# Kernel optimization log

Hardware: AMD Instinct MI355X
Metric: run time of the kernel (lower is better)

## Reference

```python
import jax, jax.numpy as jnp
import numpy as np

EMBED_DIM = 1024
HEAD_DIM = 128


def setup_inputs() -> dict:
    key = jax.random.key(0)
    k_x, k_qkv, k_out, k_b = jax.random.split(key, 4)
    x = jax.random.normal(k_x, (4, 4096, EMBED_DIM), dtype=jnp.float32)
    # torch Linear weights, stored as [in, out] so y = x @ W
    w_qkv = jax.random.normal(k_qkv, (EMBED_DIM, 3 * HEAD_DIM), dtype=jnp.float32) * (EMBED_DIM ** -0.5)
    w_out = jax.random.normal(k_out, (HEAD_DIM, EMBED_DIM), dtype=jnp.float32) * (HEAD_DIM ** -0.5)
    b_out = jax.random.normal(k_b, (EMBED_DIM,), dtype=jnp.float32) * 0.01
    return {"x": x, "w_qkv": w_qkv, "w_out": w_out, "b_out": b_out}


def reference(x, w_qkv, w_out, b_out):
    b, t, c = x.shape
    qkv = x @ w_qkv                                  # [b, t, 3*head_dim]
    q, k, v = jnp.split(qkv, 3, axis=-1)             # each [b, t, head_dim]
    # NOTE: original scales by embed_dim**-0.5 (c), not head_dim**-0.5
    wei = jnp.einsum('bqd,bkd->bqk', q, k) * (c ** -0.5)  # [b, t, t]
    causal = jnp.tril(jnp.ones((t, t), dtype=bool))
    wei = jnp.where(causal, wei, -jnp.inf)
    wei = jax.nn.softmax(wei, axis=-1)
    out = jnp.einsum('bqk,bkd->bqd', wei, v)         # [b, t, head_dim]
    return out @ w_out + b_out                       # [b, t, embed_dim]
```

## Files before the change

kernel.cpp:

```cpp
#include <hip/hip_runtime.h>
#include <hip/hip_bf16.h>

typedef __attribute__((ext_vector_type(8))) short short8;
typedef __attribute__((ext_vector_type(4))) float float4v;

#define AS1(p) ((const __attribute__((address_space(1))) void*)(p))
#define AS3(p) ((__attribute__((address_space(3))) void*)(p))

#define NSPLIT 8

__device__ __forceinline__ ushort f2bf(float f) {
    union { float f; unsigned u; } v; v.f = f;
    unsigned u = v.u;
    unsigned r = (u + 0x7fffu + ((u >> 16) & 1u)) >> 16;
    return (ushort)r;
}
__device__ __forceinline__ ushort f2bf_trunc(float f) {
    union { float f; unsigned u; } v; v.f = f;
    return (ushort)(v.u >> 16);
}
__device__ __forceinline__ float bf2f(ushort u) {
    union { unsigned u; float f; } v; v.u = ((unsigned)u) << 16;
    return v.f;
}

__global__ void transpose_cast(const float* __restrict__ in, ushort* __restrict__ out, int R, int C) {
    int idx = blockIdx.x * blockDim.x + threadIdx.x;
    if (idx >= R * C) return;
    int r = idx / C, c = idx - r * C;
    out[(size_t)c * R + r] = f2bf(in[idx]);
}

__device__ __forceinline__ void stage128x64(const ushort* gbase, int ld, ushort* lds, int tid) {
    const int wavebase = tid & 192;
#pragma unroll
    for (int j = 0; j < 4; ++j) {
        int idx = j * 256 + tid;
        int row = idx >> 3;
        int slot = idx & 7;
        int s = slot ^ (row & 7);
        const ushort* g = gbase + (size_t)row * ld + s * 8;
        int ldsoff = (j * 256 + wavebase) * 16;
        __builtin_amdgcn_global_load_lds(AS1(g), AS3((char*)lds + ldsoff), 16, 0, 0);
    }
}

__device__ __forceinline__ void compute64(const ushort* As, const ushort* Bs,
                                          int wr, int wc, int row16, int grp,
                                          float4v acc[4][4]) {
    const char* Ab = (const char*)As;
    const char* Bb = (const char*)Bs;
#pragma unroll
    for (int kk = 0; kk < 2; ++kk) {
        short8 a[4], b[4];
        const int sw = row16 & 7;
#pragma unroll
        for (int m = 0; m < 4; ++m)
            a[m] = *(const short8*)(Ab + (wr * 64 + m * 16 + row16) * 128 + (((kk * 4 + grp) ^ sw) << 4));
#pragma unroll
        for (int n = 0; n < 4; ++n)
            b[n] = *(const short8*)(Bb + (wc * 64 + n * 16 + row16) * 128 + (((kk * 4 + grp) ^ sw) << 4));
#pragma unroll
        for (int m = 0; m < 4; ++m)
#pragma unroll
            for (int n = 0; n < 4; ++n)
                acc[m][n] = __builtin_amdgcn_mfma_f32_16x16x32_bf16(a[m], b[n], acc[m][n], 0, 0, 0);
    }
}

__device__ __forceinline__ void compute64x128(const ushort* As, const ushort* Bs,
                                              int wr, int wc, int row16, int grp,
                                              float4v acc[2][4]) {
    const char* Ab = (const char*)As;
    const char* Bb = (const char*)Bs;
#pragma unroll
    for (int kk = 0; kk < 2; ++kk) {
        short8 a[2], b[4];
        const int sw = row16 & 7;
#pragma unroll
        for (int m = 0; m < 2; ++m)
            a[m] = *(const short8*)(Ab + (wr * 32 + m * 16 + row16) * 128 + (((kk * 4 + grp) ^ sw) << 4));
#pragma unroll
        for (int n = 0; n < 4; ++n)
            b[n] = *(const short8*)(Bb + (wc * 64 + n * 16 + row16) * 128 + (((kk * 4 + grp) ^ sw) << 4));
#pragma unroll
        for (int m = 0; m < 2; ++m)
#pragma unroll
            for (int n = 0; n < 4; ++n)
                acc[m][n] = __builtin_amdgcn_mfma_f32_16x16x32_bf16(a[m], b[n], acc[m][n], 0, 0, 0);
    }
}

__global__ __launch_bounds__(256) void gemm_qkv(const float* __restrict__ x,
                                                const ushort* __restrict__ wT,
                                                ushort* __restrict__ Qm,
                                                ushort* __restrict__ Km,
                                                ushort* __restrict__ Vt) {
    __shared__ ushort S[12288];
    ushort* As = S;
    ushort* Bs = S + 4096;
    const int tid = threadIdx.x;
    const int lane = tid & 63, w = tid >> 6;
    const int row16 = lane & 15, grp = lane >> 4;
    const int wr = w >> 1, wc = w & 1;
    const int mt = blockIdx.x * 64;
    const int by = blockIdx.y;
    const int n0 = by * 128;

    float4v acc[2][4];
#pragma unroll
    for (int m = 0; m < 2; ++m)
#pragma unroll
        for (int n = 0; n < 4; ++n) acc[m][n] = (float4v){0.f, 0.f, 0.f, 0.f};

#define LOAD_A(KT)                                                         \
    _Pragma("unroll") for (int j = 0; j < 2; ++j) {                        \
        int idx = j * 256 + tid;                                           \
        int row = idx >> 3, slot = idx & 7;                                \
        const float* src = x + (size_t)(mt + row) * 1024 + (KT) + slot * 8;\
        va[j][0] = *(const float4*)(src);                                  \
        va[j][1] = *(const float4*)(src + 4);                              \
    }

    float4 va[2][2];
    LOAD_A(0);

    for (int kt = 0; kt < 1024; kt += 64) {
        stage128x64(wT + (size_t)n0 * 1024 + kt, 1024, Bs, tid);
#pragma unroll
        for (int j = 0; j < 2; ++j) {
            int idx = j * 256 + tid;
            int row = idx >> 3, slot = idx & 7;
            short8 h;
            h[0] = f2bf(va[j][0].x); h[1] = f2bf(va[j][0].y);
            h[2] = f2bf(va[j][0].z); h[3] = f2bf(va[j][0].w);
            h[4] = f2bf(va[j][1].x); h[5] = f2bf(va[j][1].y);
            h[6] = f2bf(va[j][1].z); h[7] = f2bf(va[j][1].w);
            *(short8*)((char*)As + row * 128 + ((slot ^ (row & 7)) << 4)) = h;
        }
        __syncthreads();
        if (kt + 64 < 1024) LOAD_A(kt + 64);
        compute64x128(As, Bs, wr, wc, row16, grp, acc);
        __syncthreads();
    }
#undef LOAD_A

    if (by == 2) {
#pragma unroll
        for (int m = 0; m < 2; ++m)
#pragma unroll
            for (int i = 0; i < 4; ++i) {
                int trow = wr * 32 + m * 16 + grp * 4 + i;
#pragma unroll
                for (int n = 0; n < 4; ++n) {
                    int d = wc * 64 + n * 16 + row16;
                    S[d * 72 + trow] = f2bf(acc[m][n][i]);
                }
            }
        __syncthreads();
        const int b = mt >> 12, tloc = mt & 4095;
#pragma unroll
        for (int j = 0; j < 4; ++j) {
            int chunk = j * 256 + tid;
            int d = chunk >> 3, tc = chunk & 7;
            *(short8*)(Vt + ((size_t)(b * 128 + d)) * 4096 + tloc + tc * 8) =
                *(const short8*)(S + d * 72 + tc * 8);
        }
        return;
    }

    const float oscale = (by == 0) ? (0.03125f * 1.44269504f) : 1.0f;
    ushort* dst = (by == 0) ? Qm : Km;
#pragma unroll
    for (int m = 0; m < 2; ++m)
#pragma unroll
        for (int i = 0; i < 4; ++i) {
            int row = mt + wr * 32 + m * 16 + grp * 4 + i;
#pragma unroll
            for (int n = 0; n < 4; ++n) {
                int coll = wc * 64 + n * 16 + row16;
                dst[(size_t)row * 128 + coll] = f2bf(acc[m][n][i] * oscale);
            }
        }
}

__global__ __launch_bounds__(256, 3) void attn_split(const ushort* __restrict__ Qm,
                                                     const ushort* __restrict__ Km,
                                                     const ushort* __restrict__ Vt,
                                                     ushort* __restrict__ Opart,
                                                     float* __restrict__ Lpart) {
    __shared__ ushort Ks[2][32 * 128];
    __shared__ ushort Vs[2][128 * 32];
    __shared__ ushort Ps[4][32 * 32];

    const int tid = threadIdx.x;
    const int lane = tid & 63, w = tid >> 6;
    const int row16 = lane & 15, grp = lane >> 4;

    const int bx = blockIdx.x;
    const int xcd = bx & 7;
    const int b = xcd >> 1;
    const int combo = ((bx >> 3) << 1) | (xcd & 1);
    const int qb = 31 - (combo >> 3);
    const int s = combo & 7;

    const int ext = 4 * qb + 4;
    const int t0 = (s * ext) >> 3;
    const int t1 = ((s + 1) * ext) >> 3;

    const int qtile32 = qb * 4 + w;
    const int qt0 = qtile32 * 32;
    const int qmax = qt0 + 31;
    const size_t pbase = ((size_t)b * 128 + qtile32) * NSPLIT + s;
    float* mlL = Lpart + pbase * 32;

    if (t0 >= t1) {
        if (lane < 32) mlL[lane] = 0.f;
        return;
    }

    const ushort* qbp = Qm + ((size_t)(b * 4096 + qt0 + row16)) * 128 + grp * 8;
    short8 qf[2][4];
#pragma unroll
    for (int rt = 0; rt < 2; ++rt)
#pragma unroll
        for (int kk = 0; kk < 4; ++kk)
            qf[rt][kk] = *reinterpret_cast<const short8*>(qbp + rt * 16 * 128 + kk * 32);

    float4v o[2][8];
#pragma unroll
    for (int rt = 0; rt < 2; ++rt)
#pragma unroll
        for (int dt = 0; dt < 8; ++dt) o[rt][dt] = (float4v){0.f, 0.f, 0.f, 0.f};
    float lrun[2][4];
#pragma unroll
    for (int rt = 0; rt < 2; ++rt)
#pragma unroll
        for (int i = 0; i < 4; ++i) lrun[rt][i] = 0.f;

    const ushort* kbase = Km + (size_t)b * 4096 * 128;
    const ushort* vbase = Vt + (size_t)b * 128 * 4096;
    char* Pw = (char*)&Ps[w][0];

#define STAGE_KV(KVT, BUF)                                                                     \
    {                                                                                          \
        const ushort* kb_ = kbase + (size_t)(KVT) * 128;                                       \
        _Pragma("unroll") for (int j = 0; j < 2; ++j) {                                        \
            int idx = j * 256 + tid;                                                           \
            int row = idx >> 4, c = idx & 15;                                                  \
            int sc_ = (c & 8) | ((c & 7) ^ (row & 7));                                         \
            __builtin_amdgcn_global_load_lds(AS1(kb_ + (size_t)row * 128 + sc_ * 8),           \
                AS3((char*)&Ks[BUF][0] + (j * 256 + (tid & 192)) * 16), 16, 0, 0);             \
        }                                                                                      \
        const ushort* vb_ = vbase + (KVT);                                                     \
        _Pragma("unroll") for (int j = 0; j < 2; ++j) {                                        \
            int idx = j * 256 + tid;                                                           \
            int row = idx >> 2, c = idx & 3;                                                   \
            int sc_ = c ^ ((row >> 1) & 3);                                                    \
            __builtin_amdgcn_global_load_lds(AS1(vb_ + (size_t)row * 4096 + sc_ * 8),          \
                AS3((char*)&Vs[BUF][0] + (j * 256 + (tid & 192)) * 16), 16, 0, 0);             \
        }                                                                                      \
    }

    STAGE_KV(t0 * 32, 0);

    int cur = 0;
    for (int t = t0; t < t1; ++t) {
        const int kvt = t * 32;
        __builtin_amdgcn_s_barrier();
        if (t + 1 < t1) {
            STAGE_KV((t + 1) * 32, cur ^ 1);
            asm volatile("s_waitcnt vmcnt(4)" ::: "memory");
        } else {
            asm volatile("s_waitcnt vmcnt(0)" ::: "memory");
        }
        __builtin_amdgcn_s_barrier();
        __builtin_amdgcn_sched_barrier(0);

        if (kvt <= qmax) {
            float4v a[2][2];
#pragma unroll
            for (int rt = 0; rt < 2; ++rt)
#pragma unroll
                for (int ct = 0; ct < 2; ++ct) a[rt][ct] = (float4v){0.f, 0.f, 0.f, 0.f};
            const char* Kb = (const char*)&Ks[cur][0];
            __builtin_amdgcn_s_setprio(1);
#pragma unroll
            for (int ct = 0; ct < 2; ++ct) {
                int r0 = ct * 16 + row16;
                int rx = r0 & 7;
#pragma unroll
                for (int kk = 0; kk < 4; ++kk) {
                    int c = kk * 4 + grp;
                    int sc_ = (c & 8) | ((c & 7) ^ rx);
                    short8 kfr = *(const short8*)(Kb + r0 * 256 + sc_ * 16);
                    a[0][ct] = __builtin_amdgcn_mfma_f32_16x16x32_bf16(qf[0][kk], kfr, a[0][ct], 0, 0, 0);
                    a[1][ct] = __builtin_amdgcn_mfma_f32_16x16x32_bf16(qf[1][kk], kfr, a[1][ct], 0, 0, 0);
                }
            }
            __builtin_amdgcn_s_setprio(0);
            if (kvt + 31 > qt0) {
#pragma unroll
                for (int ct = 0; ct < 2; ++ct) {
                    int kcol = kvt + ct * 16 + row16;
#pragma unroll
                    for (int rt = 0; rt < 2; ++rt)
#pragma unroll
                        for (int i = 0; i < 4; ++i) {
                            int q = qt0 + rt * 16 + grp * 4 + i;
                            if (kcol > q) a[rt][ct][i] = -3e38f;
                        }
                }
            }
#pragma unroll
            for (int rt = 0; rt < 2; ++rt)
#pragma unroll
                for (int i = 0; i < 4; ++i) {
#pragma unroll
                    for (int ct = 0; ct < 2; ++ct) {
                        float p = exp2f(a[rt][ct][i]);
                        a[rt][ct][i] = p;
                        lrun[rt][i] += p;
                    }
                }
#pragma unroll
            for (int rt = 0; rt < 2; ++rt)
#pragma unroll
                for (int ct = 0; ct < 2; ++ct)
#pragma unroll
                    for (int i = 0; i < 4; ++i) {
                        int r = rt * 16 + grp * 4 + i;
                        int chunk = (ct * 2 + (row16 >> 3)) ^ ((r >> 1) & 3);
                        *(ushort*)(Pw + r * 64 + (chunk << 4) + ((row16 & 7) << 1)) = f2bf_trunc(a[rt][ct][i]);
                    }
            const char* Vb = (const char*)&Vs[cur][0];
            __builtin_amdgcn_s_setprio(1);
            {
                short8 pa0 = *(const short8*)(Pw + row16 * 64 + ((grp ^ ((row16 >> 1) & 3)) << 4));
                short8 pa1 = *(const short8*)(Pw + (16 + row16) * 64 + ((grp ^ (((16 + row16) >> 1) & 3)) << 4));
#pragma unroll
                for (int dt = 0; dt < 8; ++dt) {
                    int r = dt * 16 + row16;
                    int sc_ = grp ^ ((r >> 1) & 3);
                    short8 vfr = *(const short8*)(Vb + r * 64 + sc_ * 16);
                    o[0][dt] = __builtin_amdgcn_mfma_f32_16x16x32_bf16(pa0, vfr, o[0][dt], 0, 0, 0);
                    o[1][dt] = __builtin_amdgcn_mfma_f32_16x16x32_bf16(pa1, vfr, o[1][dt], 0, 0, 0);
                }
            }
            __builtin_amdgcn_s_setprio(0);
        }
        cur ^= 1;
    }
#undef STAGE_KV

#pragma unroll
    for (int rt = 0; rt < 2; ++rt)
#pragma unroll
        for (int i = 0; i < 4; ++i) {
            float psum = lrun[rt][i];
#pragma unroll
            for (int msk = 1; msk < 16; msk <<= 1) psum += __shfl_xor(psum, msk);
            lrun[rt][i] = psum;
        }
    ushort* ob = Opart + pbase * 32 * 128;
#pragma unroll
    for (int rt = 0; rt < 2; ++rt)
#pragma unroll
        for (int i = 0; i < 4; ++i) {
            int r = rt * 16 + grp * 4 + i;
#pragma unroll
            for (int dt = 0; dt < 8; ++dt)
                ob[(size_t)r * 128 + dt * 16 + row16] = f2bf(o[rt][dt][i]);
        }
    if (row16 == 0) {
#pragma unroll
        for (int rt = 0; rt < 2; ++rt)
#pragma unroll
            for (int i = 0; i < 4; ++i)
                mlL[rt * 16 + grp * 4 + i] = lrun[rt][i];
    }
}

__global__ __launch_bounds__(128) void attn_combine(const ushort* __restrict__ Opart,
                                                    const float* __restrict__ Lpart,
                                                    ushort* __restrict__ AO) {
    const int row = blockIdx.x;
    const int b = row >> 12, t = row & 4095;
    const int qtile = t >> 5, r = t & 31;
    const size_t sb = (((size_t)b * 128 + qtile) * NSPLIT);
    const int col = threadIdx.x;
    float acc = 0.f, denom = 0.f;
#pragma unroll
    for (int s = 0; s < NSPLIT; ++s) {
        float l = Lpart[(sb + s) * 32 + r];
        if (l > 0.f) {
            denom += l;
            acc += bf2f(Opart[((sb + s) * 32 + r) * 128 + col]);
        }
    }
    AO[(size_t)row * 128 + col] = f2bf(acc / denom);
}

__global__ __launch_bounds__(256) void gemm_out(const ushort* __restrict__ AO,
                                                const ushort* __restrict__ wT,
                                                const float* __restrict__ bias,
                                                float* __restrict__ out) {
    __shared__ ushort As[128 * 64];
    __shared__ ushort Bs[128 * 64];
    const int tid = threadIdx.x;
    const int lane = tid & 63, w = tid >> 6;
    const int row16 = lane & 15, grp = lane >> 4;
    const int wr = w >> 1, wc = w & 1;
    const int mt = blockIdx.x * 128;
    const int n0 = blockIdx.y * 128;

    float4v acc[4][4];
#pragma unroll
    for (int m = 0; m < 4; ++m)
#pragma unroll
        for (int n = 0; n < 4; ++n) acc[m][n] = (float4v){0.f, 0.f, 0.f, 0.f};

#pragma unroll
    for (int kt = 0; kt < 128; kt += 64) {
        stage128x64(AO + (size_t)mt * 128 + kt, 128, As, tid);
        stage128x64(wT + (size_t)n0 * 128 + kt, 128, Bs, tid);
        __syncthreads();
        compute64(As, Bs, wr, wc, row16, grp, acc);
        __syncthreads();
    }

#pragma unroll
    for (int n = 0; n < 4; ++n) {
        int col = n0 + wc * 64 + n * 16 + row16;
        float bv = bias[col];
#pragma unroll
        for (int m = 0; m < 4; ++m)
#pragma unroll
            for (int i = 0; i < 4; ++i) {
                int row = mt + wr * 64 + m * 16 + grp * 4 + i;
                out[(size_t)row * 1024 + col] = acc[m][n][i] + bv;
            }
    }
}

extern "C" void kernel_launch(void* const* d_in, const int* in_sizes, int n_in,
                              void* d_out, int out_size, void* d_ws, size_t ws_size,
                              hipStream_t stream) {
    const float* x     = (const float*)d_in[0];
    const float* w_qkv = (const float*)d_in[1];
    const float* w_out = (const float*)d_in[2];
    const float* b_out = (const float*)d_in[3];
    float* out = (float*)d_out;

    char* ws = (char*)d_ws;
    ushort* wqkvT = (ushort*)(ws + 33554432);
    ushort* woutT = (ushort*)(ws + 34340864);
    ushort* Qm    = (ushort*)(ws + 34603008);
    ushort* Km    = (ushort*)(ws + 38797312);
    ushort* Vt    = (ushort*)(ws + 42991616);
    ushort* AO    = (ushort*)(ws + 47185920);
    ushort* Opart = (ushort*)(ws);
    float* Lpart  = (float*)(ws + 51380224);

    transpose_cast<<<dim3((1024 * 384 + 255) / 256), dim3(256), 0, stream>>>(w_qkv, wqkvT, 1024, 384);
    transpose_cast<<<dim3((128 * 1024 + 255) / 256), dim3(256), 0, stream>>>(w_out, woutT, 128, 1024);

    gemm_qkv<<<dim3(256, 3), dim3(256), 0, stream>>>(x, wqkvT, Qm, Km, Vt);

    attn_split<<<dim3(1024), dim3(256), 0, stream>>>(Qm, Km, Vt, Opart, Lpart);
    attn_combine<<<dim3(16384), dim3(128), 0, stream>>>(Opart, Lpart, AO);

    gemm_out<<<dim3(128, 8), dim3(256), 0, stream>>>(AO, woutT, b_out, out);
}
```

Baseline: 108.6 us.

## Use 32x32x16 MFMA with transposed S and register-only P handoff

Measured after the change: 105.3 us. 1.03x faster.

```diff
diff --git a/kernel.cpp b/kernel.cpp
--- a/kernel.cpp
+++ b/kernel.cpp
@@ -3,6 +3,8 @@
 
 typedef __attribute__((ext_vector_type(8))) short short8;
 typedef __attribute__((ext_vector_type(4))) float float4v;
+typedef __attribute__((ext_vector_type(16))) float f32x16;
+typedef __attribute__((ext_vector_type(4))) unsigned uint4v;
 
 #define AS1(p) ((const __attribute__((address_space(1))) void*)(p))
 #define AS3(p) ((__attribute__((address_space(3))) void*)(p))
@@ -14,10 +16,6 @@
     unsigned u = v.u;
     unsigned r = (u + 0x7fffu + ((u >> 16) & 1u)) >> 16;
     return (ushort)r;
-}
-__device__ __forceinline__ ushort f2bf_trunc(float f) {
-    union { float f; unsigned u; } v; v.f = f;
-    return (ushort)(v.u >> 16);
 }
 __device__ __forceinline__ float bf2f(ushort u) {
     union { unsigned u; float f; } v; v.u = ((unsigned)u) << 16;
@@ -191,11 +189,11 @@
                                                      float* __restrict__ Lpart) {
     __shared__ ushort Ks[2][32 * 128];
     __shared__ ushort Vs[2][128 * 32];
-    __shared__ ushort Ps[4][32 * 32];
 
     const int tid = threadIdx.x;
     const int lane = tid & 63, w = tid >> 6;
-    const int row16 = lane & 15, grp = lane >> 4;
+    const int key31 = lane & 31;
+    const int g = lane >> 5;
 
     const int bx = blockIdx.x;
     const int xcd = bx & 7;
@@ -219,28 +217,22 @@
         return;
     }
 
-    const ushort* qbp = Qm + ((size_t)(b * 4096 + qt0 + row16)) * 128 + grp * 8;
-    short8 qf[2][4];
-#pragma unroll
-    for (int rt = 0; rt < 2; ++rt)
-#pragma unroll
-        for (int kk = 0; kk < 4; ++kk)
-            qf[rt][kk] = *reinterpret_cast<const short8*>(qbp + rt * 16 * 128 + kk * 32);
-
-    float4v o[2][8];
-#pragma unroll
-    for (int rt = 0; rt < 2; ++rt)
-#pragma unroll
-        for (int dt = 0; dt < 8; ++dt) o[rt][dt] = (float4v){0.f, 0.f, 0.f, 0.f};
-    float lrun[2][4];
-#pragma unroll
-    for (int rt = 0; rt < 2; ++rt)
-#pragma unroll
-        for (int i = 0; i < 4; ++i) lrun[rt][i] = 0.f;
+    const int qrow = qt0 + key31;
+    const ushort* qbp = Qm + ((size_t)(b * 4096 + qrow)) * 128 + g * 8;
+    short8 qf[8];
+#pragma unroll
+    for (int sl = 0; sl < 8; ++sl)
+        qf[sl] = *reinterpret_cast<const short8*>(qbp + sl * 16);
+
+    f32x16 o[4];
+#pragma unroll
+    for (int d4 = 0; d4 < 4; ++d4)
+#pragma unroll
+        for (int r = 0; r < 16; ++r) o[d4][r] = 0.f;
+    float lrun = 0.f;
 
     const ushort* kbase = Km + (size_t)b * 4096 * 128;
     const ushort* vbase = Vt + (size_t)b * 128 * 4096;
-    char* Pw = (char*)&Ps[w][0];
 
 #define STAGE_KV(KVT, BUF)                                                                     \
     {                                                                                          \
@@ -278,74 +270,60 @@
         __builtin_amdgcn_sched_barrier(0);
 
         if (kvt <= qmax) {
-            float4v a[2][2];
-#pragma unroll
-            for (int rt = 0; rt < 2; ++rt)
-#pragma unroll
-                for (int ct = 0; ct < 2; ++ct) a[rt][ct] = (float4v){0.f, 0.f, 0.f, 0.f};
             const char* Kb = (const char*)&Ks[cur][0];
+            f32x16 st;
+#pragma unroll
+            for (int r = 0; r < 16; ++r) st[r] = 0.f;
             __builtin_amdgcn_s_setprio(1);
 #pragma unroll
-            for (int ct = 0; ct < 2; ++ct) {
-                int r0 = ct * 16 + row16;
-                int rx = r0 & 7;
-#pragma unroll
-                for (int kk = 0; kk < 4; ++kk) {
-                    int c = kk * 4 + grp;
-                    int sc_ = (c & 8) | ((c & 7) ^ rx);
-                    short8 kfr = *(const short8*)(Kb + r0 * 256 + sc_ * 16);
-                    a[0][ct] = __builtin_amdgcn_mfma_f32_16x16x32_bf16(qf[0][kk], kfr, a[0][ct], 0, 0, 0);
-                    a[1][ct] = __builtin_amdgcn_mfma_f32_16x16x32_bf16(qf[1][kk], kfr, a[1][ct], 0, 0, 0);
-                }
+            for (int sl = 0; sl < 8; ++sl) {
+                int c = sl * 2 + g;
+                int sc_ = (c & 8) | ((c & 7) ^ (key31 & 7));
+                short8 kfr = *(const short8*)(Kb + key31 * 256 + sc_ * 16);
+                st = __builtin_amdgcn_mfma_f32_32x32x16_bf16(kfr, qf[sl], st, 0, 0, 0);
             }
             __builtin_amdgcn_s_setprio(0);
             if (kvt + 31 > qt0) {
 #pragma unroll
-                for (int ct = 0; ct < 2; ++ct) {
-                    int kcol = kvt + ct * 16 + row16;
-#pragma unroll
-                    for (int rt = 0; rt < 2; ++rt)
-#pragma unroll
-                        for (int i = 0; i < 4; ++i) {
-                            int q = qt0 + rt * 16 + grp * 4 + i;
-                            if (kcol > q) a[rt][ct][i] = -3e38f;
-                        }
+                for (int r = 0; r < 16; ++r) {
+                    int key = kvt + (r & 3) + 8 * (r >> 2) + 4 * g;
+                    if (key > qrow) st[r] = -3e38f;
                 }
             }
 #pragma unroll
-            for (int rt = 0; rt < 2; ++rt)
-#pragma unroll
-                for (int i = 0; i < 4; ++i) {
-#pragma unroll
-                    for (int ct = 0; ct < 2; ++ct) {
-                        float p = exp2f(a[rt][ct][i]);
-                        a[rt][ct][i] = p;
-                        lrun[rt][i] += p;
-                    }
-                }
-#pragma unroll
-            for (int rt = 0; rt < 2; ++rt)
-#pragma unroll
-                for (int ct = 0; ct < 2; ++ct)
-#pragma unroll
-                    for (int i = 0; i < 4; ++i) {
-                        int r = rt * 16 + grp * 4 + i;
-                        int chunk = (ct * 2 + (row16 >> 3)) ^ ((r >> 1) & 3);
-                        *(ushort*)(Pw + r * 64 + (chunk << 4) + ((row16 & 7) << 1)) = f2bf_trunc(a[rt][ct][i]);
-                    }
+            for (int r = 0; r < 16; ++r) {
+                float p = exp2f(st[r]);
+                st[r] = p;
+                lrun += p;
+            }
+            unsigned pk0, pk1, pk2, pk3, pk4, pk5, pk6, pk7;
+            asm("v_cvt_pk_bf16_f32 %0, %1, %2" : "=v"(pk0) : "v"(st[0]),  "v"(st[1]));
+            asm("v_cvt_pk_bf16_f32 %0, %1, %2" : "=v"(pk1) : "v"(st[2]),  "v"(st[3]));
+            asm("v_cvt_pk_bf16_f32 %0, %1, %2" : "=v"(pk2) : "v"(st[4]),  "v"(st[5]));
+            asm("v_cvt_pk_bf16_f32 %0, %1, %2" : "=v"(pk3) : "v"(st[6]),  "v"(st[7]));
+            asm("v_cvt_pk_bf16_f32 %0, %1, %2" : "=v"(pk4) : "v"(st[8]),  "v"(st[9]));
+            asm("v_cvt_pk_bf16_f32 %0, %1, %2" : "=v"(pk5) : "v"(st[10]), "v"(st[11]));
+            asm("v_cvt_pk_bf16_f32 %0, %1, %2" : "=v"(pk6) : "v"(st[12]), "v"(st[13]));
+            asm("v_cvt_pk_bf16_f32 %0, %1, %2" : "=v"(pk7) : "v"(st[14]), "v"(st[15]));
+            asm volatile("v_permlane32_swap_b32 %0, %1" : "+v"(pk0), "+v"(pk2));
+            asm volatile("v_permlane32_swap_b32 %0, %1" : "+v"(pk1), "+v"(pk3));
+            asm volatile("v_permlane32_swap_b32 %0, %1" : "+v"(pk4), "+v"(pk6));
+            asm volatile("v_permlane32_swap_b32 %0, %1" : "+v"(pk5), "+v"(pk7));
+            union FW { uint4v u; short8 s; };
+            FW f0; f0.u = (uint4v){pk0, pk1, pk2, pk3};
+            FW f1; f1.u = (uint4v){pk4, pk5, pk6, pk7};
+            short8 fa0 = f0.s;
+            short8 fa1 = f1.s;
             const char* Vb = (const char*)&Vs[cur][0];
             __builtin_amdgcn_s_setprio(1);
-            {
-                short8 pa0 = *(const short8*)(Pw + row16 * 64 + ((grp ^ ((row16 >> 1) & 3)) << 4));
-                short8 pa1 = *(const short8*)(Pw + (16 + row16) * 64 + ((grp ^ (((16 + row16) >> 1) & 3)) << 4));
-#pragma unroll
-                for (int dt = 0; dt < 8; ++dt) {
-                    int r = dt * 16 + row16;
-                    int sc_ = grp ^ ((r >> 1) & 3);
-                    short8 vfr = *(const short8*)(Vb + r * 64 + sc_ * 16);
-                    o[0][dt] = __builtin_amdgcn_mfma_f32_16x16x32_bf16(pa0, vfr, o[0][dt], 0, 0, 0);
-                    o[1][dt] = __builtin_amdgcn_mfma_f32_16x16x32_bf16(pa1, vfr, o[1][dt], 0, 0, 0);
-                }
+#pragma unroll
+            for (int d4 = 0; d4 < 4; ++d4) {
+                int d = d4 * 32 + key31;
+                int sw = (d >> 1) & 3;
+                short8 v0 = *(const short8*)(Vb + d * 64 + ((0 * 2 + g) ^ sw) * 16);
+                o[d4] = __builtin_amdgcn_mfma_f32_32x32x16_bf16(fa0, v0, o[d4], 0, 0, 0);
+                short8 v1 = *(const short8*)(Vb + d * 64 + ((1 * 2 + g) ^ sw) * 16);
+                o[d4] = __builtin_amdgcn_mfma_f32_32x32x16_bf16(fa1, v1, o[d4], 0, 0, 0);
             }
             __builtin_amdgcn_s_setprio(0);
         }
@@ -353,32 +331,16 @@
     }
 #undef STAGE_KV
 
-#pragma unroll
-    for (int rt = 0; rt < 2; ++rt)
-#pragma unroll
-        for (int i = 0; i < 4; ++i) {
-            float psum = lrun[rt][i];
-#pragma unroll
-            for (int msk = 1; msk < 16; msk <<= 1) psum += __shfl_xor(psum, msk);
-            lrun[rt][i] = psum;
-        }
+    lrun += __shfl_xor(lrun, 32);
     ushort* ob = Opart + pbase * 32 * 128;
 #pragma unroll
-    for (int rt = 0; rt < 2; ++rt)
-#pragma unroll
-        for (int i = 0; i < 4; ++i) {
-            int r = rt * 16 + grp * 4 + i;
-#pragma unroll
-            for (int dt = 0; dt < 8; ++dt)
-                ob[(size_t)r * 128 + dt * 16 + row16] = f2bf(o[rt][dt][i]);
-        }
-    if (row16 == 0) {
-#pragma unroll
-        for (int rt = 0; rt < 2; ++rt)
-#pragma unroll
-            for (int i = 0; i < 4; ++i)
-                mlL[rt * 16 + grp * 4 + i] = lrun[rt][i];
-    }
+    for (int d4 = 0; d4 < 4; ++d4)
+#pragma unroll
+        for (int r = 0; r < 16; ++r) {
+            int qr = (r & 3) + 8 * (r >> 2) + 4 * g;
+            ob[(size_t)qr * 128 + d4 * 32 + key31] = f2bf(o[d4][r]);
+        }
+    if (lane < 32) mlL[lane] = lrun;
 }
 
 __global__ __launch_bounds__(128) void attn_combine(const ushort* __restrict__ Opart,
```
